# Optimization experiments

Hardware: AMD Instinct MI355X
Metric: run time of the kernel (lower is better)

The kernel has to match this reference:

```python
import jax, jax.numpy as jnp
import numpy as np

N = 50000        # nodes
E_RAND = 800000  # random edges; self-loops appended -> E = E_RAND + N
H = 4            # heads
D_IN = 256
D_HID = 64       # per-head hidden (H*D_HID == D_IN -> identity residual in layer 1)
D_OUT = 32       # classes per head
SLOPE = 0.2      # leaky-relu negative slope


def setup_inputs() -> dict:
    key = jax.random.key(0)
    ks = jax.random.split(key, 13)
    loops = jnp.arange(N, dtype=jnp.int32)
    src = jnp.concatenate([jax.random.randint(ks[0], (E_RAND,), 0, N, dtype=jnp.int32), loops])
    dst = jnp.concatenate([jax.random.randint(ks[1], (E_RAND,), 0, N, dtype=jnp.int32), loops])
    h = jax.random.normal(ks[2], (N, D_IN), dtype=jnp.float32)
    def w(k, shape, fan):
        return jax.random.normal(k, shape, dtype=jnp.float32) * (1.0 / np.sqrt(fan))
    return {
        "h": h, "src": src, "dst": dst,
        # layer 1 (tuple in_feats -> separate fc_src / fc_dst in dgl GATConv)
        "W1_src": w(ks[3], (D_IN, H * D_HID), D_IN),
        "W1_dst": w(ks[4], (D_IN, H * D_HID), D_IN),
        "al1": w(ks[5], (H, D_HID), D_HID),
        "ar1": w(ks[6], (H, D_HID), D_HID),
        # layer 2
        "W2_src": w(ks[7], (H * D_HID, H * D_OUT), H * D_HID),
        "W2_dst": w(ks[8], (H * D_HID, H * D_OUT), H * D_HID),
        "al2": w(ks[9], (H, D_OUT), D_OUT),
        "ar2": w(ks[10], (H, D_OUT), D_OUT),
        # residual projection for layer 2 (in_dim != heads*out)
        "Wres2": w(ks[11], (H * D_HID, H * D_OUT), H * D_HID),
    }


def gat_conv(h_node, src, dst, Ws, Wd, al, ar, heads, dout, resval):
    n = h_node.shape[0]
    fs = (h_node @ Ws).reshape(n, heads, dout)   # [N,H,D] projected src feats
    fd = (h_node @ Wd).reshape(n, heads, dout)
    el = jnp.sum(fs * al, axis=-1)               # [N,H]
    er = jnp.sum(fd * ar, axis=-1)               # [N,H]
    e = jax.nn.leaky_relu(el[src] + er[dst], SLOPE)           # [E,H] edge scores
    emax = jax.ops.segment_max(e, dst, num_segments=n)        # segment softmax over dst
    ex = jnp.exp(e - emax[dst])
    denom = jax.ops.segment_sum(ex, dst, num_segments=n)
    a = ex / denom[dst]                                        # [E,H] attention
    msg = fs[src] * a[:, :, None]                              # [E,H,D] gather * weight
    out = jax.ops.segment_sum(msg, dst, num_segments=n)       # [N,H,D] scatter-add
    return out + resval


def reference(h, src, dst, W1_src, W1_dst, al1, ar1, W2_src, W2_dst, al2, ar2, Wres2):
    # layer 1: identity residual (in_dim == heads*hidden), elu activation, flatten heads
    res1 = h.reshape(-1, H, D_HID)
    h1 = gat_conv(h, src, dst, W1_src, W1_dst, al1, ar1, H, D_HID, res1)
    h1 = jax.nn.elu(h1).reshape(-1, H * D_HID)
    # layer 2: linear residual, no activation, mean over heads
    res2 = (h1 @ Wres2).reshape(-1, H, D_OUT)
    h2 = gat_conv(h1, src, dst, W2_src, W2_dst, al2, ar2, H, D_OUT, res2)
    return h2.mean(axis=1)                                     # [N, num_classes]
```

## Files before the change

kernel.cpp:

```cpp
#include <hip/hip_runtime.h>
#include <hip/hip_bf16.h>

#define NN 50000
#define EE 850000
#define NBLK_SCAN 98

typedef unsigned short u16;
using short8 = __attribute__((ext_vector_type(8))) short;
using f32x4  = __attribute__((ext_vector_type(4))) float;

__device__ __forceinline__ float bf2f(u16 u) {
    union { unsigned int i; float f; } v; v.i = ((unsigned int)u) << 16; return v.f;
}
__device__ __forceinline__ u16 f2bf(float f) {
    __hip_bfloat16 h = __float2bfloat16(f);
    return *reinterpret_cast<u16*>(&h);
}

__device__ __forceinline__ float ld1(const void* X, size_t i, bool f32m) {
    return f32m ? ((const float*)X)[i] : bf2f(((const u16*)X)[i]);
}
__device__ __forceinline__ void load4(const void* X, size_t g, bool f32m, float o[4]) {
    if (f32m) {
        float4 v = ((const float4*)X)[g];
        o[0] = v.x; o[1] = v.y; o[2] = v.z; o[3] = v.w;
    } else {
        ushort4 v = ((const ushort4*)X)[g];
        o[0] = bf2f(v.x); o[1] = bf2f(v.y); o[2] = bf2f(v.z); o[3] = bf2f(v.w);
    }
}

__global__ void k_detect(const u16* __restrict__ hh, int* __restrict__ flag,
                         int* __restrict__ deg) {
    if (blockIdx.x != 0) {
        int i = (blockIdx.x - 1) * 256 + threadIdx.x;
        if (i < NN) deg[i] = 0;
        return;
    }
    __shared__ int sm[256];
    int t = threadIdx.x;
    int c = 0;
    for (int i = 0; i < 16; ++i) {
        u16 u = hh[t * 16 + i];
        int e = (u >> 7) & 0xFF;
        if (e != 0 && (e < 90 || e > 160)) ++c;
    }
    sm[t] = c;
    __syncthreads();
    for (int s = 128; s > 0; s >>= 1) {
        if (t < s) sm[t] += sm[t + s];
        __syncthreads();
    }
    if (t == 0) *flag = (sm[0] > 200) ? 1 : 0;
}

__global__ void k_prep(const void* __restrict__ W1s, const void* __restrict__ al1,
                       const void* __restrict__ W1d, const void* __restrict__ ar1,
                       const void* __restrict__ W2s, const void* __restrict__ al2,
                       const void* __restrict__ W2d, const void* __restrict__ ar2,
                       const void* __restrict__ Wres2, const int* __restrict__ dst,
                       u16* __restrict__ BT1, u16* __restrict__ BT2,
                       float* __restrict__ wl1, float* __restrict__ wr1,
                       float* __restrict__ wl2, float* __restrict__ wr2,
                       int* __restrict__ deg, int* __restrict__ eorder,
                       const int* __restrict__ mode) {
    int bid = blockIdx.x;
    if (bid >= 528) {
        int e = (bid - 528) * 256 + threadIdx.x;
        if (e < EE) {
            int r = atomicAdd(&deg[dst[e]], 1);
            eorder[e] = r;
        }
        return;
    }
    bool f32m = (*mode) != 0;
    if (bid < 512) {
        int id = bid * 256 + threadIdx.x;
        int which = id >> 16;
        int rem = id & 65535;
        int n = rem >> 8, k = rem & 255;
        if (which == 0) {
            BT1[n * 256 + k] = f2bf(ld1(W1s, (size_t)k * 256 + n, f32m));
        } else {
            float v = (n < 128) ? ld1(W2s, (size_t)k * 128 + n, f32m)
                                : ld1(Wres2, (size_t)k * 128 + (n - 128), f32m);
            BT2[n * 256 + k] = f2bf(v);
        }
    } else {
        int id = (bid - 512) * 256 + threadIdx.x;
        int which = id >> 10;
        int rem = id & 1023;
        int k = rem >> 2, h = rem & 3;
        float s = 0.f;
        if (which == 0) {
            for (int d = 0; d < 64; ++d) s += ld1(W1s, k * 256 + h * 64 + d, f32m) * ld1(al1, h * 64 + d, f32m);
            wl1[k * 4 + h] = s;
        } else if (which == 1) {
            for (int d = 0; d < 64; ++d) s += ld1(W1d, k * 256 + h * 64 + d, f32m) * ld1(ar1, h * 64 + d, f32m);
            wr1[k * 4 + h] = s;
        } else if (which == 2) {
            for (int d = 0; d < 32; ++d) s += ld1(W2s, k * 128 + h * 32 + d, f32m) * ld1(al2, h * 32 + d, f32m);
            wl2[k * 4 + h] = s;
        } else {
            for (int d = 0; d < 32; ++d) s += ld1(W2d, k * 128 + h * 32 + d, f32m) * ld1(ar2, h * 32 + d, f32m);
            wr2[k * 4 + h] = s;
        }
    }
}

__global__ void k_scan1(const int* __restrict__ deg, int* __restrict__ rowptr,
                        int* __restrict__ bsum) {
    __shared__ int sm[512];
    int t = threadIdx.x;
    int i = blockIdx.x * 512 + t;
    int v = (i < NN) ? deg[i] : 0;
    int x = v;
    sm[t] = x;
    __syncthreads();
    for (int off = 1; off < 512; off <<= 1) {
        int y = (t >= off) ? sm[t - off] : 0;
        __syncthreads();
        x += y;
        sm[t] = x;
        __syncthreads();
    }
    if (i < NN) rowptr[i] = x - v;
    if (t == 511) bsum[blockIdx.x] = x;
}

__global__ void k_scan3_eler1(int* __restrict__ rowptr, const int* __restrict__ bsum,
                              const void* __restrict__ X,
                              const float* __restrict__ wl, const float* __restrict__ wr,
                              float* __restrict__ el, float* __restrict__ er,
                              const int* __restrict__ mode) {
    int bid = blockIdx.x;
    if (bid < 196) {
        __shared__ int sm[NBLK_SCAN];
        int t = threadIdx.x;
        if (t < NBLK_SCAN) sm[t] = bsum[t];
        __syncthreads();
        int g = bid >> 1;
        int pre = 0;
        for (int j = 0; j < g; ++j) pre += sm[j];
        int i = bid * 256 + t;
        if (i < NN) {
            rowptr[i] += pre;
            if (i == 0) rowptr[NN] = EE;
        }
        return;
    }
    bool f32m = (*mode) != 0;
    int wave = threadIdx.x >> 6, lane = threadIdx.x & 63;
    int node = (bid - 196) * 4 + wave;
    float a[4];
    load4(X, (size_t)node * 64 + lane, f32m, a);
    float accl[4] = {0, 0, 0, 0}, accr[4] = {0, 0, 0, 0};
    int k0 = lane * 4;
#pragma unroll
    for (int j = 0; j < 4; ++j) {
        float4 wlv = ((const float4*)wl)[k0 + j];
        float4 wrv = ((const float4*)wr)[k0 + j];
        accl[0] += a[j] * wlv.x; accl[1] += a[j] * wlv.y;
        accl[2] += a[j] * wlv.z; accl[3] += a[j] * wlv.w;
        accr[0] += a[j] * wrv.x; accr[1] += a[j] * wrv.y;
        accr[2] += a[j] * wrv.z; accr[3] += a[j] * wrv.w;
    }
#pragma unroll
    for (int off = 32; off > 0; off >>= 1) {
#pragma unroll
        for (int t = 0; t < 4; ++t) {
            accl[t] += __shfl_down(accl[t], off, 64);
            accr[t] += __shfl_down(accr[t], off, 64);
        }
    }
    if (lane == 0) {
        float4 vl = {accl[0], accl[1], accl[2], accl[3]};
        float4 vr = {accr[0], accr[1], accr[2], accr[3]};
        ((float4*)el)[node] = vl;
        ((float4*)er)[node] = vr;
    }
}

__global__ void k_awgen(const int* __restrict__ src, const int* __restrict__ dst,
                        const int* __restrict__ eorder, const int* __restrict__ rowptr,
                        const float* __restrict__ el, const float* __restrict__ er,
                        u16* __restrict__ aw, int* __restrict__ csrc, int writeCsrc) {
    int e = blockIdx.x * 256 + threadIdx.x;
    if (e >= EE) return;
    int s = src[e], d = dst[e];
    int slot = rowptr[d] + eorder[e];
    if (writeCsrc) csrc[slot] = s;
    float4 eL = ((const float4*)el)[s];
    float4 eR = ((const float4*)er)[d];
    float ev[4] = {eL.x + eR.x, eL.y + eR.y, eL.z + eR.z, eL.w + eR.w};
    ushort4 o;
    u16* op = (u16*)&o;
#pragma unroll
    for (int t = 0; t < 4; ++t) {
        float x = ev[t];
        x = x > 0.f ? x : 0.2f * x;
        x = fminf(fmaxf(x, -60.f), 60.f);
        op[t] = f2bf(__expf(x));
    }
    ((ushort4*)aw)[slot] = o;
}

__global__ void k_gemm_mfma(const void* __restrict__ A, int aDual,
                            const u16* __restrict__ BT, u16* __restrict__ C,
                            const int* __restrict__ mode) {
    bool af32 = aDual && ((*mode) != 0);
    __shared__ u16 smem[128 * 72 * 2];
    u16* At = smem;
    u16* Bt = smem + 128 * 72;
    int t = threadIdx.x;
    int lane = t & 63, w = t >> 6;
    int mt = blockIdx.x >> 1, nt = blockIdx.x & 1;
    int m0 = mt * 128, n0 = nt * 128;
    int wr = (w >> 1) * 64, wc = (w & 1) * 64;
    f32x4 acc[4][4] = {};
    int q = lane >> 4, cl = lane & 15;

    for (int ph = 0; ph < 4; ++ph) {
        int kb = ph * 64;
        for (int it = 0; it < 4; ++it) {
            int c = it * 256 + t;
            int row = c >> 3, c8 = c & 7;
            int rowg = m0 + row;
            if (af32) {
                if (rowg < NN) {
                    const float* ap = (const float*)A + (size_t)rowg * 256 + kb + c8 * 8;
                    float4 v0 = ((const float4*)ap)[0];
                    float4 v1 = ((const float4*)ap)[1];
                    ushort4 lo = {f2bf(v0.x), f2bf(v0.y), f2bf(v0.z), f2bf(v0.w)};
                    ushort4 hi = {f2bf(v1.x), f2bf(v1.y), f2bf(v1.z), f2bf(v1.w)};
                    *(ushort4*)&At[row * 72 + c8 * 8] = lo;
                    *(ushort4*)&At[row * 72 + c8 * 8 + 4] = hi;
                } else {
                    ushort4 z = {0, 0, 0, 0};
                    *(ushort4*)&At[row * 72 + c8 * 8] = z;
                    *(ushort4*)&At[row * 72 + c8 * 8 + 4] = z;
                }
            } else {
                float4 av;
                if (rowg < NN) {
                    av = *(const float4*)((const u16*)A + (size_t)rowg * 256 + kb + c8 * 8);
                } else {
                    av = make_float4(0.f, 0.f, 0.f, 0.f);
                }
                *(float4*)&At[row * 72 + c8 * 8] = av;
            }
            float4 bv = *(const float4*)(BT + (size_t)(n0 + row) * 256 + kb + c8 * 8);
            *(float4*)&Bt[row * 72 + c8 * 8] = bv;
        }
        __syncthreads();
#pragma unroll
        for (int ks = 0; ks < 2; ++ks) {
            short8 af[4], bf[4];
#pragma unroll
            for (int i = 0; i < 4; ++i)
                af[i] = *(const short8*)&At[(wr + i * 16 + cl) * 72 + ks * 32 + q * 8];
#pragma unroll
            for (int j = 0; j < 4; ++j)
                bf[j] = *(const short8*)&Bt[(wc + j * 16 + cl) * 72 + ks * 32 + q * 8];
#pragma unroll
            for (int i = 0; i < 4; ++i)
#pragma unroll
                for (int j = 0; j < 4; ++j)
                    acc[i][j] = __builtin_amdgcn_mfma_f32_16x16x32_bf16(af[i], bf[j], acc[i][j], 0, 0, 0);
        }
        __syncthreads();
    }
    u16* Ct = smem;
    int sw_w = q << 1;
#pragma unroll
    for (int i = 0; i < 4; ++i)
#pragma unroll
        for (int j = 0; j < 4; ++j) {
            int colb = wc + j * 16 + cl;
            int chunk = (colb >> 3) ^ sw_w;
#pragma unroll
            for (int r = 0; r < 4; ++r) {
                int row = wr + i * 16 + q * 4 + r;
                Ct[row * 128 + chunk * 8 + (colb & 7)] = f2bf(acc[i][j][r]);
            }
        }
    __syncthreads();
#pragma unroll
    for (int it = 0; it < 8; ++it) {
        int c = it * 256 + t;
        int row = c >> 4, k16 = c & 15;
        int mrow = m0 + row;
        if (mrow < NN) {
            int phys = k16 ^ (((row >> 2) & 3) << 1);
            float4 v = *(const float4*)&Ct[row * 128 + phys * 8];
            *(float4*)&C[(size_t)mrow * 256 + n0 + k16 * 8] = v;
        }
    }
}

__global__ void k_agg1(const int* __restrict__ rowptr, const int* __restrict__ csrc,
                       const u16* __restrict__ aw, const u16* __restrict__ fs,
                       const void* __restrict__ h_in, u16* __restrict__ h1,
                       const float* __restrict__ wl2, const float* __restrict__ wr2,
                       float* __restrict__ el2, float* __restrict__ er2,
                       const int* __restrict__ mode) {
    bool f32m = (*mode) != 0;
    int wave = threadIdx.x >> 6, lane = threadIdx.x & 63;
    int node = blockIdx.x * 4 + wave;
    int beg = rowptr[node], end = rowptr[node + 1];
    int head = lane >> 4;
    float a0 = 0.f, a1 = 0.f, a2 = 0.f, a3 = 0.f, ll = 0.f;
    for (int p = beg; p < end; p += 8) {
#pragma unroll
        for (int u = 0; u < 8; ++u) {
            int pp = p + u;
            int pc = pp < end ? pp : end - 1;
            int s = csrc[pc];
            float pw = bf2f(aw[(size_t)pc * 4 + head]);
            if (pp >= end) pw = 0.f;
            ushort4 fv = *(const ushort4*)(fs + (size_t)s * 256 + lane * 4);
            ll += pw;
            a0 += pw * bf2f(fv.x);
            a1 += pw * bf2f(fv.y);
            a2 += pw * bf2f(fv.z);
            a3 += pw * bf2f(fv.w);
        }
    }
    float rinv = 1.f / ll;
    float res[4];
    load4(h_in, (size_t)node * 64 + lane, f32m, res);
    float v0 = a0 * rinv + res[0], v1 = a1 * rinv + res[1];
    float v2 = a2 * rinv + res[2], v3 = a3 * rinv + res[3];
    v0 = v0 > 0.f ? v0 : __expf(v0) - 1.f;
    v1 = v1 > 0.f ? v1 : __expf(v1) - 1.f;
    v2 = v2 > 0.f ? v2 : __expf(v2) - 1.f;
    v3 = v3 > 0.f ? v3 : __expf(v3) - 1.f;
    ushort4 o = {f2bf(v0), f2bf(v1), f2bf(v2), f2bf(v3)};
    ((ushort4*)h1)[(size_t)node * 64 + lane] = o;
    float4 w0 = ((const float4*)wl2)[lane * 4 + 0];
    float4 w1 = ((const float4*)wl2)[lane * 4 + 1];
    float4 w2 = ((const float4*)wl2)[lane * 4 + 2];
    float4 w3 = ((const float4*)wl2)[lane * 4 + 3];
    float4 r0 = ((const float4*)wr2)[lane * 4 + 0];
    float4 r1 = ((const float4*)wr2)[lane * 4 + 1];
    float4 r2 = ((const float4*)wr2)[lane * 4 + 2];
    float4 r3 = ((const float4*)wr2)[lane * 4 + 3];
    float acl[4], acr[4];
    acl[0] = v0 * w0.x + v1 * w1.x + v2 * w2.x + v3 * w3.x;
    acl[1] = v0 * w0.y + v1 * w1.y + v2 * w2.y + v3 * w3.y;
    acl[2] = v0 * w0.z + v1 * w1.z + v2 * w2.z + v3 * w3.z;
    acl[3] = v0 * w0.w + v1 * w1.w + v2 * w2.w + v3 * w3.w;
    acr[0] = v0 * r0.x + v1 * r1.x + v2 * r2.x + v3 * r3.x;
    acr[1] = v0 * r0.y + v1 * r1.y + v2 * r2.y + v3 * r3.y;
    acr[2] = v0 * r0.z + v1 * r1.z + v2 * r2.z + v3 * r3.z;
    acr[3] = v0 * r0.w + v1 * r1.w + v2 * r2.w + v3 * r3.w;
#pragma unroll
    for (int off = 32; off > 0; off >>= 1) {
#pragma unroll
        for (int t = 0; t < 4; ++t) {
            acl[t] += __shfl_down(acl[t], off, 64);
            acr[t] += __shfl_down(acr[t], off, 64);
        }
    }
    if (lane == 0) {
        float4 vl = {acl[0], acl[1], acl[2], acl[3]};
        float4 vr = {acr[0], acr[1], acr[2], acr[3]};
        ((float4*)el2)[node] = vl;
        ((float4*)er2)[node] = vr;
    }
}

__global__ void k_agg2(const int* __restrict__ rowptr, const int* __restrict__ csrc,
                       const u16* __restrict__ aw, const u16* __restrict__ c2,
                       void* __restrict__ out, const int* __restrict__ mode) {
    bool f32m = (*mode) != 0;
    int wave = threadIdx.x >> 6, lane = threadIdx.x & 63;
    int node = blockIdx.x * 4 + wave;
    int beg = rowptr[node], end = rowptr[node + 1];
    int head = lane >> 4;
    float a0 = 0.f, a1 = 0.f, ll = 0.f;
    for (int p = beg; p < end; p += 8) {
#pragma unroll
        for (int u = 0; u < 8; ++u) {
            int pp = p + u;
            int pc = pp < end ? pp : end - 1;
            int s = csrc[pc];
            float pw = bf2f(aw[(size_t)pc * 4 + head]);
            if (pp >= end) pw = 0.f;
            ushort2 fv = *(const ushort2*)(c2 + (size_t)s * 256 + lane * 2);
            ll += pw;
            a0 += pw * bf2f(fv.x);
            a1 += pw * bf2f(fv.y);
        }
    }
    float rinv = 1.f / ll;
    ushort2 rv = *(const ushort2*)(c2 + (size_t)node * 256 + 128 + lane * 2);
    float o0 = a0 * rinv + bf2f(rv.x);
    float o1 = a1 * rinv + bf2f(rv.y);
    o0 += __shfl_xor(o0, 16, 64); o0 += __shfl_xor(o0, 32, 64);
    o1 += __shfl_xor(o1, 16, 64); o1 += __shfl_xor(o1, 32, 64);
    if (lane < 16) {
        float v0 = 0.25f * o0, v1 = 0.25f * o1;
        size_t oi = (size_t)node * 32 + lane * 2;
        if (f32m) {
            ((float*)out)[oi] = v0;
            ((float*)out)[oi + 1] = v1;
        } else {
            ushort2 ov = {f2bf(v0), f2bf(v1)};
            *(ushort2*)((u16*)out + oi) = ov;
        }
    }
}

extern "C" void kernel_launch(void* const* d_in, const int* in_sizes, int n_in,
                              void* d_out, int out_size, void* d_ws, size_t ws_size,
                              hipStream_t stream) {
    int ih = 0, isrc = 1, idst = 2, iW1s = 3, iW1d = 4, ial1 = 5, iar1 = 6,
        iW2s = 7, iW2d = 8, ial2 = 9, iar2 = 10, iWres = 11;
    if (n_in >= 12 && in_sizes[0] != 12800000) {
        iW1d = 0; iW1s = 1; iW2d = 2; iW2s = 3; iWres = 4; ial1 = 5; ial2 = 6;
        iar1 = 7; iar2 = 8; idst = 9; ih = 10; isrc = 11;
    }
    const void* h     = d_in[ih];
    const int* src    = (const int*)d_in[isrc];
    const int* dst    = (const int*)d_in[idst];
    const void* W1s   = d_in[iW1s];
    const void* W1d   = d_in[iW1d];
    const void* al1   = d_in[ial1];
    const void* ar1   = d_in[iar1];
    const void* W2s   = d_in[iW2s];
    const void* W2d   = d_in[iW2d];
    const void* al2   = d_in[ial2];
    const void* ar2   = d_in[iar2];
    const void* Wres2 = d_in[iWres];

    char* w = (char*)d_ws;
    size_t off = 0;
    auto alloc = [&](size_t bytes) -> void* {
        void* p = w + off;
        off += (bytes + 255) & ~(size_t)255;
        return p;
    };
    int* mode   = (int*)alloc(256);
    float* wl1 = (float*)alloc(256 * 4 * 4);
    float* wr1 = (float*)alloc(256 * 4 * 4);
    float* wl2 = (float*)alloc(256 * 4 * 4);
    float* wr2 = (float*)alloc(256 * 4 * 4);
    int* deg    = (int*)alloc(NN * 4);
    int* rowptr = (int*)alloc((NN + 1) * 4);
    int* bsum   = (int*)alloc(NBLK_SCAN * 4);
    int* eorder = (int*)alloc((size_t)EE * 4);
    int* csrc   = (int*)alloc((size_t)EE * 4);
    u16* aw     = (u16*)alloc((size_t)EE * 4 * 2);
    float* el1  = (float*)alloc((size_t)NN * 4 * 4);
    float* er1  = (float*)alloc((size_t)NN * 4 * 4);
    float* el2  = (float*)alloc((size_t)NN * 4 * 4);
    float* er2  = (float*)alloc((size_t)NN * 4 * 4);
    u16* BT1    = (u16*)alloc(256 * 256 * 2);
    u16* BT2    = (u16*)alloc(256 * 256 * 2);
    u16* fs1    = (u16*)alloc((size_t)NN * 256 * 2);
    u16* h1     = (u16*)alloc((size_t)NN * 256 * 2);
    u16* c2     = fs1;

    k_detect<<<197, 256, 0, stream>>>((const u16*)h, mode, deg);
    k_prep<<<528 + (EE + 255) / 256, 256, 0, stream>>>(
        W1s, al1, W1d, ar1, W2s, al2, W2d, ar2, Wres2, dst,
        BT1, BT2, wl1, wr1, wl2, wr2, deg, eorder, mode);
    k_scan1<<<NBLK_SCAN, 512, 0, stream>>>(deg, rowptr, bsum);
    k_scan3_eler1<<<196 + NN / 4, 256, 0, stream>>>(rowptr, bsum,
                                                    h, wl1, wr1, el1, er1, mode);
    k_awgen<<<(EE + 255) / 256, 256, 0, stream>>>(src, dst, eorder, rowptr,
                                                  el1, er1, aw, csrc, 1);
    k_gemm_mfma<<<782, 256, 0, stream>>>(h, 1, BT1, fs1, mode);
    k_agg1<<<NN / 4, 256, 0, stream>>>(rowptr, csrc, aw, fs1, h, h1,
                                       wl2, wr2, el2, er2, mode);
    k_gemm_mfma<<<782, 256, 0, stream>>>(h1, 0, BT2, c2, mode);
    k_awgen<<<(EE + 255) / 256, 256, 0, stream>>>(src, dst, eorder, rowptr,
                                                  el2, er2, aw, csrc, 0);
    k_agg2<<<NN / 4, 256, 0, stream>>>(rowptr, csrc, aw, c2, d_out, mode);
}
```

Before: 385.9 us.

## Pack edge source and attention weights into one meta record; pre-convert input to bf16

Edge source indices and the four per-head bf16 attention weights are now written as a single 16-byte record per CSR slot, so each aggregation step does one vector load instead of two scattered loads. The aggregation loops drop the padded 8-wide tail handling in favour of a plain unrolled loop. The layer-1 input is converted to bf16 once in the el/er kernel and reused by the GEMM and the residual, removing the fp32/bf16 mode branches. The h1 buffer now overwrites that bf16 copy in place. The cost is more edge-metadata bytes (16 instead of 12 per edge, 4 of them padding), and the second awgen pass now rewrites the source indices as well.

```diff
diff --git a/kernel.cpp b/kernel.cpp
--- a/kernel.cpp
+++ b/kernel.cpp
@@ -129,7 +129,7 @@
 }
 
 __global__ void k_scan3_eler1(int* __restrict__ rowptr, const int* __restrict__ bsum,
-                              const void* __restrict__ X,
+                              const void* __restrict__ X, u16* __restrict__ hb,
                               const float* __restrict__ wl, const float* __restrict__ wr,
                               float* __restrict__ el, float* __restrict__ er,
                               const int* __restrict__ mode) {
@@ -154,6 +154,8 @@
     int node = (bid - 196) * 4 + wave;
     float a[4];
     load4(X, (size_t)node * 64 + lane, f32m, a);
+    ushort4 hv = {f2bf(a[0]), f2bf(a[1]), f2bf(a[2]), f2bf(a[3])};
+    ((ushort4*)hb)[(size_t)node * 64 + lane] = hv;
     float accl[4] = {0, 0, 0, 0}, accr[4] = {0, 0, 0, 0};
     int k0 = lane * 4;
 #pragma unroll
@@ -184,17 +186,15 @@
 __global__ void k_awgen(const int* __restrict__ src, const int* __restrict__ dst,
                         const int* __restrict__ eorder, const int* __restrict__ rowptr,
                         const float* __restrict__ el, const float* __restrict__ er,
-                        u16* __restrict__ aw, int* __restrict__ csrc, int writeCsrc) {
+                        uint4* __restrict__ meta) {
     int e = blockIdx.x * 256 + threadIdx.x;
     if (e >= EE) return;
     int s = src[e], d = dst[e];
     int slot = rowptr[d] + eorder[e];
-    if (writeCsrc) csrc[slot] = s;
     float4 eL = ((const float4*)el)[s];
     float4 eR = ((const float4*)er)[d];
     float ev[4] = {eL.x + eR.x, eL.y + eR.y, eL.z + eR.z, eL.w + eR.w};
-    ushort4 o;
-    u16* op = (u16*)&o;
+    u16 op[4];
 #pragma unroll
     for (int t = 0; t < 4; ++t) {
         float x = ev[t];
@@ -202,13 +202,16 @@
         x = fminf(fmaxf(x, -60.f), 60.f);
         op[t] = f2bf(__expf(x));
     }
-    ((ushort4*)aw)[slot] = o;
-}
-
-__global__ void k_gemm_mfma(const void* __restrict__ A, int aDual,
-                            const u16* __restrict__ BT, u16* __restrict__ C,
-                            const int* __restrict__ mode) {
-    bool af32 = aDual && ((*mode) != 0);
+    uint4 m;
+    m.x = (unsigned int)s;
+    m.y = (unsigned int)op[0] | ((unsigned int)op[1] << 16);
+    m.z = (unsigned int)op[2] | ((unsigned int)op[3] << 16);
+    m.w = 0u;
+    meta[slot] = m;
+}
+
+__global__ void k_gemm_mfma(const u16* __restrict__ A,
+                            const u16* __restrict__ BT, u16* __restrict__ C) {
     __shared__ u16 smem[128 * 72 * 2];
     u16* At = smem;
     u16* Bt = smem + 128 * 72;
@@ -226,29 +229,13 @@
             int c = it * 256 + t;
             int row = c >> 3, c8 = c & 7;
             int rowg = m0 + row;
-            if (af32) {
-                if (rowg < NN) {
-                    const float* ap = (const float*)A + (size_t)rowg * 256 + kb + c8 * 8;
-                    float4 v0 = ((const float4*)ap)[0];
-                    float4 v1 = ((const float4*)ap)[1];
-                    ushort4 lo = {f2bf(v0.x), f2bf(v0.y), f2bf(v0.z), f2bf(v0.w)};
-                    ushort4 hi = {f2bf(v1.x), f2bf(v1.y), f2bf(v1.z), f2bf(v1.w)};
-                    *(ushort4*)&At[row * 72 + c8 * 8] = lo;
-                    *(ushort4*)&At[row * 72 + c8 * 8 + 4] = hi;
-                } else {
-                    ushort4 z = {0, 0, 0, 0};
-                    *(ushort4*)&At[row * 72 + c8 * 8] = z;
-                    *(ushort4*)&At[row * 72 + c8 * 8 + 4] = z;
-                }
+            float4 av;
+            if (rowg < NN) {
+                av = *(const float4*)(A + (size_t)rowg * 256 + kb + c8 * 8);
             } else {
-                float4 av;
-                if (rowg < NN) {
-                    av = *(const float4*)((const u16*)A + (size_t)rowg * 256 + kb + c8 * 8);
-                } else {
-                    av = make_float4(0.f, 0.f, 0.f, 0.f);
-                }
-                *(float4*)&At[row * 72 + c8 * 8] = av;
+                av = make_float4(0.f, 0.f, 0.f, 0.f);
             }
+            *(float4*)&At[row * 72 + c8 * 8] = av;
             float4 bv = *(const float4*)(BT + (size_t)(n0 + row) * 256 + kb + c8 * 8);
             *(float4*)&Bt[row * 72 + c8 * 8] = bv;
         }
@@ -298,45 +285,39 @@
     }
 }
 
-__global__ void k_agg1(const int* __restrict__ rowptr, const int* __restrict__ csrc,
-                       const u16* __restrict__ aw, const u16* __restrict__ fs,
-                       const void* __restrict__ h_in, u16* __restrict__ h1,
+__global__ void k_agg1(const int* __restrict__ rowptr, const uint4* __restrict__ meta,
+                       const u16* __restrict__ fs, u16* __restrict__ hb,
                        const float* __restrict__ wl2, const float* __restrict__ wr2,
-                       float* __restrict__ el2, float* __restrict__ er2,
-                       const int* __restrict__ mode) {
-    bool f32m = (*mode) != 0;
+                       float* __restrict__ el2, float* __restrict__ er2) {
     int wave = threadIdx.x >> 6, lane = threadIdx.x & 63;
     int node = blockIdx.x * 4 + wave;
     int beg = rowptr[node], end = rowptr[node + 1];
     int head = lane >> 4;
+    int hs2 = head & 2, hs1 = head & 1;
     float a0 = 0.f, a1 = 0.f, a2 = 0.f, a3 = 0.f, ll = 0.f;
-    for (int p = beg; p < end; p += 8) {
-#pragma unroll
-        for (int u = 0; u < 8; ++u) {
-            int pp = p + u;
-            int pc = pp < end ? pp : end - 1;
-            int s = csrc[pc];
-            float pw = bf2f(aw[(size_t)pc * 4 + head]);
-            if (pp >= end) pw = 0.f;
-            ushort4 fv = *(const ushort4*)(fs + (size_t)s * 256 + lane * 4);
-            ll += pw;
-            a0 += pw * bf2f(fv.x);
-            a1 += pw * bf2f(fv.y);
-            a2 += pw * bf2f(fv.z);
-            a3 += pw * bf2f(fv.w);
-        }
+#pragma unroll 8
+    for (int p = beg; p < end; ++p) {
+        uint4 mv = meta[p];
+        int s = (int)mv.x;
+        unsigned int wp = hs2 ? mv.z : mv.y;
+        float pw = bf2f(hs1 ? (u16)(wp >> 16) : (u16)wp);
+        ushort4 fv = *(const ushort4*)(fs + (size_t)s * 256 + lane * 4);
+        ll += pw;
+        a0 += pw * bf2f(fv.x);
+        a1 += pw * bf2f(fv.y);
+        a2 += pw * bf2f(fv.z);
+        a3 += pw * bf2f(fv.w);
     }
     float rinv = 1.f / ll;
-    float res[4];
-    load4(h_in, (size_t)node * 64 + lane, f32m, res);
-    float v0 = a0 * rinv + res[0], v1 = a1 * rinv + res[1];
-    float v2 = a2 * rinv + res[2], v3 = a3 * rinv + res[3];
+    ushort4 rv = ((const ushort4*)hb)[(size_t)node * 64 + lane];
+    float v0 = a0 * rinv + bf2f(rv.x), v1 = a1 * rinv + bf2f(rv.y);
+    float v2 = a2 * rinv + bf2f(rv.z), v3 = a3 * rinv + bf2f(rv.w);
     v0 = v0 > 0.f ? v0 : __expf(v0) - 1.f;
     v1 = v1 > 0.f ? v1 : __expf(v1) - 1.f;
     v2 = v2 > 0.f ? v2 : __expf(v2) - 1.f;
     v3 = v3 > 0.f ? v3 : __expf(v3) - 1.f;
     ushort4 o = {f2bf(v0), f2bf(v1), f2bf(v2), f2bf(v3)};
-    ((ushort4*)h1)[(size_t)node * 64 + lane] = o;
+    ((ushort4*)hb)[(size_t)node * 64 + lane] = o;
     float4 w0 = ((const float4*)wl2)[lane * 4 + 0];
     float4 w1 = ((const float4*)wl2)[lane * 4 + 1];
     float4 w2 = ((const float4*)wl2)[lane * 4 + 2];
@@ -370,28 +351,26 @@
     }
 }
 
-__global__ void k_agg2(const int* __restrict__ rowptr, const int* __restrict__ csrc,
-                       const u16* __restrict__ aw, const u16* __restrict__ c2,
+__global__ void k_agg2(const int* __restrict__ rowptr, const uint4* __restrict__ meta,
+                       const u16* __restrict__ c2,
                        void* __restrict__ out, const int* __restrict__ mode) {
     bool f32m = (*mode) != 0;
     int wave = threadIdx.x >> 6, lane = threadIdx.x & 63;
     int node = blockIdx.x * 4 + wave;
     int beg = rowptr[node], end = rowptr[node + 1];
     int head = lane >> 4;
+    int hs2 = head & 2, hs1 = head & 1;
     float a0 = 0.f, a1 = 0.f, ll = 0.f;
-    for (int p = beg; p < end; p += 8) {
-#pragma unroll
-        for (int u = 0; u < 8; ++u) {
-            int pp = p + u;
-            int pc = pp < end ? pp : end - 1;
-            int s = csrc[pc];
-            float pw = bf2f(aw[(size_t)pc * 4 + head]);
-            if (pp >= end) pw = 0.f;
-            ushort2 fv = *(const ushort2*)(c2 + (size_t)s * 256 + lane * 2);
-            ll += pw;
-            a0 += pw * bf2f(fv.x);
-            a1 += pw * bf2f(fv.y);
-        }
+#pragma unroll 8
+    for (int p = beg; p < end; ++p) {
+        uint4 mv = meta[p];
+        int s = (int)mv.x;
+        unsigned int wp = hs2 ? mv.z : mv.y;
+        float pw = bf2f(hs1 ? (u16)(wp >> 16) : (u16)wp);
+        ushort2 fv = *(const ushort2*)(c2 + (size_t)s * 256 + lane * 2);
+        ll += pw;
+        a0 += pw * bf2f(fv.x);
+        a1 += pw * bf2f(fv.y);
     }
     float rinv = 1.f / ll;
     ushort2 rv = *(const ushort2*)(c2 + (size_t)node * 256 + 128 + lane * 2);
@@ -450,8 +429,7 @@
     int* rowptr = (int*)alloc((NN + 1) * 4);
     int* bsum   = (int*)alloc(NBLK_SCAN * 4);
     int* eorder = (int*)alloc((size_t)EE * 4);
-    int* csrc   = (int*)alloc((size_t)EE * 4);
-    u16* aw     = (u16*)alloc((size_t)EE * 4 * 2);
+    uint4* meta = (uint4*)alloc((size_t)EE * 16);
     float* el1  = (float*)alloc((size_t)NN * 4 * 4);
     float* er1  = (float*)alloc((size_t)NN * 4 * 4);
     float* el2  = (float*)alloc((size_t)NN * 4 * 4);
@@ -459,7 +437,7 @@
     u16* BT1    = (u16*)alloc(256 * 256 * 2);
     u16* BT2    = (u16*)alloc(256 * 256 * 2);
     u16* fs1    = (u16*)alloc((size_t)NN * 256 * 2);
-    u16* h1     = (u16*)alloc((size_t)NN * 256 * 2);
+    u16* hb     = (u16*)alloc((size_t)NN * 256 * 2);
     u16* c2     = fs1;
 
     k_detect<<<197, 256, 0, stream>>>((const u16*)h, mode, deg);
@@ -468,14 +446,14 @@
         BT1, BT2, wl1, wr1, wl2, wr2, deg, eorder, mode);
     k_scan1<<<NBLK_SCAN, 512, 0, stream>>>(deg, rowptr, bsum);
     k_scan3_eler1<<<196 + NN / 4, 256, 0, stream>>>(rowptr, bsum,
-                                                    h, wl1, wr1, el1, er1, mode);
+                                                    h, hb, wl1, wr1, el1, er1, mode);
     k_awgen<<<(EE + 255) / 256, 256, 0, stream>>>(src, dst, eorder, rowptr,
-                                                  el1, er1, aw, csrc, 1);
-    k_gemm_mfma<<<782, 256, 0, stream>>>(h, 1, BT1, fs1, mode);
-    k_agg1<<<NN / 4, 256, 0, stream>>>(rowptr, csrc, aw, fs1, h, h1,
-                                       wl2, wr2, el2, er2, mode);
-    k_gemm_mfma<<<782, 256, 0, stream>>>(h1, 0, BT2, c2, mode);
+                                                  el1, er1, meta);
+    k_gemm_mfma<<<782, 256, 0, stream>>>(hb, BT1, fs1);
+    k_agg1<<<NN / 4, 256, 0, stream>>>(rowptr, meta, fs1, hb,
+                                       wl2, wr2, el2, er2);
+    k_gemm_mfma<<<782, 256, 0, stream>>>(hb, BT2, c2);
     k_awgen<<<(EE + 255) / 256, 256, 0, stream>>>(src, dst, eorder, rowptr,
-                                                  el2, er2, aw, csrc, 0);
-    k_agg2<<<NN / 4, 256, 0, stream>>>(rowptr, csrc, aw, c2, d_out, mode);
-}
+                                                  el2, er2, meta);
+    k_agg2<<<NN / 4, 256, 0, stream>>>(rowptr, meta, c2, d_out, mode);
+}
```

New measurement: 377.2 us. -2.2%, faster.
